# Performance work log

Hardware: AMD Instinct MI355X
Metric: run time of the kernel (lower is better)

Reference implementation:

```python
import jax, jax.numpy as jnp
import numpy as np

H = 8          # nheads
D_OUT = 1024   # tf_out_dim
D_HEAD = D_OUT // H
LN_EPS = 1e-5


def setup_inputs() -> dict:
    key = jax.random.key(0)
    ks = jax.random.split(key, 8)
    n_tok, d_in = 512, 1024
    return {
        "x": jax.random.normal(ks[0], (n_tok, d_in), jnp.float32),
        "c": jax.random.normal(ks[1], (H, n_tok, D_HEAD, D_HEAD), jnp.float32),
        "m_prev": jax.random.normal(ks[2], (H, n_tok, 1), jnp.float32),
        "n_prev": jax.random.normal(ks[3], (H, n_tok, D_HEAD), jnp.float32),
        "Wqkvo": jax.random.normal(ks[4], (d_in, 4 * D_OUT), jnp.float32) * 0.02,
        "bqkvo": jax.random.normal(ks[5], (4 * D_OUT,), jnp.float32) * 0.02,
        "Wuf": jax.random.normal(ks[6], (d_in, 2 * H), jnp.float32) * 0.02,
        "buf": jax.random.normal(ks[7], (2 * H,), jnp.float32) * 0.02,
    }


def reference(x, c, m_prev, n_prev, Wqkvo, bqkvo, Wuf, buf):
    n_tok = x.shape[0]
    scale = jnp.sqrt(jnp.float32(D_HEAD))  # sqrt(tf_out_dim / nheads)

    # projections: 'n (h d) -> h n d'
    qkvo = (x @ Wqkvo + bqkvo).reshape(n_tok, H, 4 * D_HEAD).transpose(1, 0, 2)
    q, k, v, o = jnp.split(qkvo, 4, axis=-1)          # each (H, n, d)
    k = k / scale

    # per-token outer-product update matrix ct = v k^T : (H, n, d, d)
    ct = v[..., :, None] * k[..., None, :]

    uf = (x @ Wuf + buf).reshape(n_tok, H, 2).transpose(1, 0, 2)  # (H, n, 2)
    u, f = uf[..., 0:1], uf[..., 1:2]                  # (H, n, 1)

    # stabilized exp gating (gate='exp', c is not None branch)
    m = jnp.maximum(f + m_prev, u)                     # (H, n, 1)
    ue = jnp.exp(u - m)
    fe = jnp.exp(f + m_prev - m)

    c_new = fe[..., None] * c + ue[..., None] * ct     # (H, n, d, d)
    n_new = fe * n_prev + ue * k                       # (H, n, d)

    # readout (note: original uses ct, not c_new, in the readout einsum)
    h = jnp.einsum('hnkl,hnl->hnk', ct, q)             # (H, n, d)
    nm = jnp.abs(jnp.einsum('hnk,hnk->hn', n_new, q))  # (H, n)
    h = h / jnp.maximum(nm, 1.0)[..., None]
    h = h * jax.nn.sigmoid(o)

    # 'h n d -> n (h d)', residual, LayerNorm over last dim (no affine)
    h = h.transpose(1, 0, 2).reshape(n_tok, D_OUT)
    h = x + h
    mu = jnp.mean(h, axis=-1, keepdims=True)
    var = jnp.var(h, axis=-1, keepdims=True)
    h = (h - mu) / jnp.sqrt(var + LN_EPS)
    return (c_new, h)
```

## Files before the change

kernel.cpp:

```cpp
#include <hip/hip_runtime.h>
#include <hip/hip_bf16.h>
#include <math.h>

#define KSCALE 0.08838834764831845f

typedef __bf16 bf16x8 __attribute__((ext_vector_type(8)));
typedef float  f32x4  __attribute__((ext_vector_type(4)));
typedef unsigned short u16x4 __attribute__((ext_vector_type(4)));
typedef unsigned short u16x8 __attribute__((ext_vector_type(8)));

__device__ inline unsigned short f2bf(float f) {
    unsigned int u = __float_as_uint(f);
    unsigned int r = (u + 0x7FFFu + ((u >> 16) & 1u)) >> 16;
    return (unsigned short)r;
}

__device__ __forceinline__ void gll16(const unsigned short* g, unsigned short* l) {
    __builtin_amdgcn_global_load_lds(
        (const __attribute__((address_space(1))) unsigned int*)g,
        (__attribute__((address_space(3))) unsigned int*)l,
        16, 0, 0);
}

__global__ __launch_bounds__(256) void prep_kernel(const float* __restrict__ x,
                                                   unsigned short* __restrict__ xb,
                                                   const float* __restrict__ W,
                                                   unsigned short* __restrict__ Wt,
                                                   const float* __restrict__ Wuf,
                                                   const float* __restrict__ buf,
                                                   const float* __restrict__ m_prev,
                                                   float* __restrict__ fe_ue) {
    int b = blockIdx.x;
    const int tid = threadIdx.x;
    if (b < 512) {
        int t = b * 256 + tid;
        float4 v = reinterpret_cast<const float4*>(x)[t];
        u16x4 o = { f2bf(v.x), f2bf(v.y), f2bf(v.z), f2bf(v.w) };
        reinterpret_cast<u16x4*>(xb)[t] = o;
    } else if (b < 1536) {
        __shared__ unsigned short tile[64][65];
        int bb = b - 512;
        int k0 = (bb & 15) * 64;
        int n0 = (bb >> 4) * 64;
        int r16 = tid >> 4, c4 = (tid & 15) * 4;
#pragma unroll
        for (int p = 0; p < 4; ++p) {
            int r = p * 16 + r16;
            float4 v = *reinterpret_cast<const float4*>(&W[(size_t)(k0 + r) * 4096 + n0 + c4]);
            tile[r][c4 + 0] = f2bf(v.x);
            tile[r][c4 + 1] = f2bf(v.y);
            tile[r][c4 + 2] = f2bf(v.z);
            tile[r][c4 + 3] = f2bf(v.w);
        }
        __syncthreads();
        int kc = (tid & 7) * 8, r32 = tid >> 3;
#pragma unroll
        for (int p = 0; p < 2; ++p) {
            int rr = p * 32 + r32;
            u16x8 o;
#pragma unroll
            for (int j = 0; j < 8; ++j) o[j] = tile[kc + j][rr];
            *reinterpret_cast<u16x8*>(&Wt[(size_t)(n0 + rr) * 1024 + k0 + kc]) = o;
        }
    } else {
        const int n = b - 1536;
        const int lane = tid & 63, w = tid >> 6;
        const float* xr = x + (size_t)n * 1024;
        float4 p = {0.f, 0.f, 0.f, 0.f};
#pragma unroll
        for (int i = 0; i < 16; ++i) {
            int k = lane + i * 64;
            float xv = xr[k];
            float4 wv = *reinterpret_cast<const float4*>(&Wuf[(size_t)k * 16 + 4 * w]);
            p.x += xv * wv.x; p.y += xv * wv.y; p.z += xv * wv.z; p.w += xv * wv.w;
        }
#pragma unroll
        for (int off = 32; off; off >>= 1) {
            p.x += __shfl_down(p.x, off);
            p.y += __shfl_down(p.y, off);
            p.z += __shfl_down(p.z, off);
            p.w += __shfl_down(p.w, off);
        }
        if (lane == 0) {
#pragma unroll
            for (int t = 0; t < 2; ++t) {
                int h = 2 * w + t;
                float u = (t ? p.z : p.x) + buf[4 * w + 2 * t];
                float f = (t ? p.w : p.y) + buf[4 * w + 2 * t + 1];
                float mp = m_prev[h * 512 + n];
                float m = fmaxf(f + mp, u);
                fe_ue[(h * 512 + n) * 2 + 0] = expf(f + mp - m);
                fe_ue[(h * 512 + n) * 2 + 1] = expf(u - m);
            }
        }
    }
}

__global__ __launch_bounds__(256) void gemm_qkvo(const unsigned short* __restrict__ A,
                                                 const unsigned short* __restrict__ Bt,
                                                 const float* __restrict__ bias,
                                                 float* __restrict__ C) {
    __shared__ __align__(16) unsigned short As[2][64 * 64];
    __shared__ __align__(16) unsigned short Bs[2][64 * 64];
    const int bn = blockIdx.x & 63;
    const int bm = blockIdx.x >> 6;
    const int m0 = bm * 64, n0 = bn * 64;
    const int tid = threadIdx.x;
    const int lane = tid & 63, wave = tid >> 6;
    const int wr = wave >> 1, wc = wave & 1;
    f32x4 acc[2][2] = {};

    const int srow = lane >> 3;
    const int scol = (lane & 7) * 8;

#pragma unroll
    for (int c = 0; c < 2; ++c) {
        int chunk = wave * 2 + c;
        int row = chunk * 8 + srow;
        gll16(A + (size_t)(m0 + row) * 1024 + scol, &As[0][chunk * 512]);
        gll16(Bt + (size_t)(n0 + row) * 1024 + scol, &Bs[0][chunk * 512]);
    }
    __syncthreads();

    int cur = 0;
    for (int t = 0; t < 16; ++t) {
        if (t < 15) {
            int k0 = (t + 1) * 64;
#pragma unroll
            for (int c = 0; c < 2; ++c) {
                int chunk = wave * 2 + c;
                int row = chunk * 8 + srow;
                gll16(A + (size_t)(m0 + row) * 1024 + k0 + scol, &As[cur ^ 1][chunk * 512]);
                gll16(Bt + (size_t)(n0 + row) * 1024 + k0 + scol, &Bs[cur ^ 1][chunk * 512]);
            }
        }
        const unsigned short* as = As[cur];
        const unsigned short* bs = Bs[cur];
        const int row = lane & 15;
        const int kof = (lane >> 4) * 8;
#pragma unroll
        for (int kk = 0; kk < 2; ++kk) {
            int kb = kk * 32 + kof;
            bf16x8 a0 = *reinterpret_cast<const bf16x8*>(&as[(wr * 32 + row) * 64 + kb]);
            bf16x8 a1 = *reinterpret_cast<const bf16x8*>(&as[(wr * 32 + 16 + row) * 64 + kb]);
            bf16x8 b0 = *reinterpret_cast<const bf16x8*>(&bs[(wc * 32 + row) * 64 + kb]);
            bf16x8 b1 = *reinterpret_cast<const bf16x8*>(&bs[(wc * 32 + 16 + row) * 64 + kb]);
            acc[0][0] = __builtin_amdgcn_mfma_f32_16x16x32_bf16(a0, b0, acc[0][0], 0, 0, 0);
            acc[0][1] = __builtin_amdgcn_mfma_f32_16x16x32_bf16(a0, b1, acc[0][1], 0, 0, 0);
            acc[1][0] = __builtin_amdgcn_mfma_f32_16x16x32_bf16(a1, b0, acc[1][0], 0, 0, 0);
            acc[1][1] = __builtin_amdgcn_mfma_f32_16x16x32_bf16(a1, b1, acc[1][1], 0, 0, 0);
        }
        __syncthreads();
        cur ^= 1;
    }

    const int cn = lane & 15, cm = (lane >> 4) * 4;
#pragma unroll
    for (int i = 0; i < 2; ++i)
#pragma unroll
        for (int j = 0; j < 2; ++j) {
            int gm = m0 + wr * 32 + i * 16 + cm;
            int gn = n0 + wc * 32 + j * 16 + cn;
            float b = bias[gn];
#pragma unroll
            for (int v = 0; v < 4; ++v)
                C[(size_t)(gm + v) * 4096 + gn] = acc[i][j][v] + b;
        }
}

__global__ __launch_bounds__(256) void fuse_main(const float* __restrict__ qkvo,
                                                 const float* __restrict__ c_in,
                                                 const float* __restrict__ n_prev,
                                                 const float* __restrict__ fe_ue,
                                                 float* __restrict__ c_out,
                                                 float* __restrict__ hst) {
    const int blk = blockIdx.x;
    const int h = blk >> 9, n = blk & 511;
    const int tid = threadIdx.x;
    __shared__ float k_s[128], v_s[128];
    __shared__ float rkq[4], rnq[4];

    const float* base = qkvo + (size_t)n * 4096 + h * 512;
    const float fe = fe_ue[(h * 512 + n) * 2 + 0];
    const float ue = fe_ue[(h * 512 + n) * 2 + 1];

    float kq_p = 0.f, nq_p = 0.f;
    if (tid < 128) {
        float q = base[tid];
        float k = base[128 + tid] * KSCALE;
        float v = base[256 + tid];
        k_s[tid] = k;
        v_s[tid] = v;
        float nn = fe * n_prev[(size_t)(h * 512 + n) * 128 + tid] + ue * k;
        kq_p = k * q;
        nq_p = nn * q;
    }
#pragma unroll
    for (int off = 32; off; off >>= 1) {
        kq_p += __shfl_down(kq_p, off);
        nq_p += __shfl_down(nq_p, off);
    }
    if ((tid & 63) == 0) { rkq[tid >> 6] = kq_p; rnq[tid >> 6] = nq_p; }
    __syncthreads();
    const float kq = rkq[0] + rkq[1];
    const float nm = fabsf(rnq[0] + rnq[1]);
    const float g = kq / fmaxf(nm, 1.0f);

    const f32x4* cin4 = reinterpret_cast<const f32x4*>(c_in + (size_t)(h * 512 + n) * 16384);
    f32x4* cout4 = reinterpret_cast<f32x4*>(c_out + (size_t)(h * 512 + n) * 16384);
#pragma unroll
    for (int it = 0; it < 16; ++it) {
        int e4 = tid + it * 256;
        int i = e4 >> 5;
        int j4 = (e4 & 31) * 4;
        f32x4 cv = __builtin_nontemporal_load(&cin4[e4]);
        float uv = ue * v_s[i];
        f32x4 o;
        o.x = fe * cv.x + uv * k_s[j4 + 0];
        o.y = fe * cv.y + uv * k_s[j4 + 1];
        o.z = fe * cv.z + uv * k_s[j4 + 2];
        o.w = fe * cv.w + uv * k_s[j4 + 3];
        __builtin_nontemporal_store(o, &cout4[e4]);
    }

    if (tid < 128) {
        float o = base[384 + tid];
        float sig = 1.f / (1.f + expf(-o));
        hst[(size_t)n * 1024 + h * 128 + tid] = v_s[tid] * g * sig;
    }
}

__global__ __launch_bounds__(256) void ln_kernel(const float* __restrict__ x,
                                                 const float* __restrict__ hst,
                                                 float* __restrict__ out) {
    int n = blockIdx.x, tid = threadIdx.x;
    float4 hv = reinterpret_cast<const float4*>(hst + (size_t)n * 1024)[tid];
    float4 xv = reinterpret_cast<const float4*>(x + (size_t)n * 1024)[tid];
    float4 s = { hv.x + xv.x, hv.y + xv.y, hv.z + xv.z, hv.w + xv.w };
    float sum = s.x + s.y + s.z + s.w;
    float sq = s.x * s.x + s.y * s.y + s.z * s.z + s.w * s.w;
#pragma unroll
    for (int off = 32; off; off >>= 1) {
        sum += __shfl_down(sum, off);
        sq += __shfl_down(sq, off);
    }
    __shared__ float rs[4], rq[4];
    if ((tid & 63) == 0) { rs[tid >> 6] = sum; rq[tid >> 6] = sq; }
    __syncthreads();
    sum = rs[0] + rs[1] + rs[2] + rs[3];
    sq = rq[0] + rq[1] + rq[2] + rq[3];
    float mu = sum * (1.f / 1024.f);
    float var = sq * (1.f / 1024.f) - mu * mu;
    float inv = rsqrtf(var + 1e-5f);
    float4 o4 = { (s.x - mu) * inv, (s.y - mu) * inv, (s.z - mu) * inv, (s.w - mu) * inv };
    reinterpret_cast<float4*>(out)[(size_t)n * 256 + tid] = o4;
}

extern "C" void kernel_launch(void* const* d_in, const int* in_sizes, int n_in,
                              void* d_out, int out_size, void* d_ws, size_t ws_size,
                              hipStream_t stream) {
    const float* x      = (const float*)d_in[0];
    const float* c_in   = (const float*)d_in[1];
    const float* m_prev = (const float*)d_in[2];
    const float* n_prev = (const float*)d_in[3];
    const float* Wqkvo  = (const float*)d_in[4];
    const float* bqkvo  = (const float*)d_in[5];
    const float* Wuf    = (const float*)d_in[6];
    const float* buf    = (const float*)d_in[7];
    float* out = (float*)d_out;
    char* ws = (char*)d_ws;

    unsigned short* xb   = (unsigned short*)(ws);
    unsigned short* Wt   = (unsigned short*)(ws + (1u << 20));
    float* qkvo          = (float*)(ws + 9u * (1u << 20));
    float* fe_ue         = (float*)(ws + 17u * (1u << 20));
    float* hst           = (float*)(ws + 17u * (1u << 20) + (1u << 16));

    prep_kernel<<<dim3(2048), dim3(256), 0, stream>>>(x, xb, Wqkvo, Wt, Wuf, buf, m_prev, fe_ue);
    gemm_qkvo  <<<dim3(512),  dim3(256), 0, stream>>>(xb, Wt, bqkvo, qkvo);
    fuse_main  <<<dim3(4096), dim3(256), 0, stream>>>(qkvo, c_in, n_prev, fe_ue, out, hst);
    ln_kernel  <<<dim3(512),  dim3(256), 0, stream>>>(x, hst, out + 67108864ull);
}
```

Measured before the change: 132.2 us.

## Split-K the QKVO GEMM and fuse LayerNorm into main kernel via counters

The projection GEMM is split into two K halves, so it launches 1024 blocks instead of 512 and writes two partial outputs. The main fused kernel sums the partials and adds the bias. The separate LayerNorm kernel is removed. The last of the 8 head-blocks for a token, found through an atomic counter, does the residual add and LayerNorm. This aims to raise GEMM occupancy and drop one launch and its tail, at the cost of extra partial-result traffic and atomic and fence overhead.

```diff
diff --git a/kernel.cpp b/kernel.cpp
--- a/kernel.cpp
+++ b/kernel.cpp
@@ -29,10 +29,12 @@
                                                    const float* __restrict__ Wuf,
                                                    const float* __restrict__ buf,
                                                    const float* __restrict__ m_prev,
-                                                   float* __restrict__ fe_ue) {
+                                                   float* __restrict__ fe_ue,
+                                                   int* __restrict__ cnt) {
     int b = blockIdx.x;
     const int tid = threadIdx.x;
     if (b < 512) {
+        if (b == 0) { cnt[tid] = 0; cnt[tid + 256] = 0; }
         int t = b * 256 + tid;
         float4 v = reinterpret_cast<const float4*>(x)[t];
         u16x4 o = { f2bf(v.x), f2bf(v.y), f2bf(v.z), f2bf(v.w) };
@@ -98,13 +100,16 @@
 
 __global__ __launch_bounds__(256) void gemm_qkvo(const unsigned short* __restrict__ A,
                                                  const unsigned short* __restrict__ Bt,
-                                                 const float* __restrict__ bias,
-                                                 float* __restrict__ C) {
+                                                 float* __restrict__ Cp) {
     __shared__ __align__(16) unsigned short As[2][64 * 64];
     __shared__ __align__(16) unsigned short Bs[2][64 * 64];
-    const int bn = blockIdx.x & 63;
-    const int bm = blockIdx.x >> 6;
+    const int kh = blockIdx.x >> 9;
+    const int t9 = blockIdx.x & 511;
+    const int bn = t9 & 63;
+    const int bm = t9 >> 6;
     const int m0 = bm * 64, n0 = bn * 64;
+    const size_t kb0 = (size_t)kh * 512;
+    float* C = Cp + (size_t)kh * (512 * 4096);
     const int tid = threadIdx.x;
     const int lane = tid & 63, wave = tid >> 6;
     const int wr = wave >> 1, wc = wave & 1;
@@ -117,15 +122,15 @@
     for (int c = 0; c < 2; ++c) {
         int chunk = wave * 2 + c;
         int row = chunk * 8 + srow;
-        gll16(A + (size_t)(m0 + row) * 1024 + scol, &As[0][chunk * 512]);
-        gll16(Bt + (size_t)(n0 + row) * 1024 + scol, &Bs[0][chunk * 512]);
+        gll16(A + (size_t)(m0 + row) * 1024 + kb0 + scol, &As[0][chunk * 512]);
+        gll16(Bt + (size_t)(n0 + row) * 1024 + kb0 + scol, &Bs[0][chunk * 512]);
     }
     __syncthreads();
 
     int cur = 0;
-    for (int t = 0; t < 16; ++t) {
-        if (t < 15) {
-            int k0 = (t + 1) * 64;
+    for (int t = 0; t < 8; ++t) {
+        if (t < 7) {
+            size_t k0 = kb0 + (t + 1) * 64;
 #pragma unroll
             for (int c = 0; c < 2; ++c) {
                 int chunk = wave * 2 + c;
@@ -161,34 +166,39 @@
         for (int j = 0; j < 2; ++j) {
             int gm = m0 + wr * 32 + i * 16 + cm;
             int gn = n0 + wc * 32 + j * 16 + cn;
-            float b = bias[gn];
 #pragma unroll
             for (int v = 0; v < 4; ++v)
-                C[(size_t)(gm + v) * 4096 + gn] = acc[i][j][v] + b;
+                C[(size_t)(gm + v) * 4096 + gn] = acc[i][j][v];
         }
 }
 
 __global__ __launch_bounds__(256) void fuse_main(const float* __restrict__ qkvo,
+                                                 const float* __restrict__ bias,
+                                                 const float* __restrict__ x,
                                                  const float* __restrict__ c_in,
                                                  const float* __restrict__ n_prev,
                                                  const float* __restrict__ fe_ue,
                                                  float* __restrict__ c_out,
-                                                 float* __restrict__ hst) {
+                                                 float* __restrict__ hst,
+                                                 int* __restrict__ cnt,
+                                                 float* __restrict__ h_out) {
     const int blk = blockIdx.x;
     const int h = blk >> 9, n = blk & 511;
     const int tid = threadIdx.x;
     __shared__ float k_s[128], v_s[128];
     __shared__ float rkq[4], rnq[4];
-
-    const float* base = qkvo + (size_t)n * 4096 + h * 512;
+    __shared__ int winflag;
+
+    const float* baseA = qkvo + (size_t)n * 4096 + h * 512;
+    const float* baseB = baseA + (size_t)512 * 4096;
     const float fe = fe_ue[(h * 512 + n) * 2 + 0];
     const float ue = fe_ue[(h * 512 + n) * 2 + 1];
 
     float kq_p = 0.f, nq_p = 0.f;
     if (tid < 128) {
-        float q = base[tid];
-        float k = base[128 + tid] * KSCALE;
-        float v = base[256 + tid];
+        float q = baseA[tid] + baseB[tid] + bias[h * 512 + tid];
+        float k = (baseA[128 + tid] + baseB[128 + tid] + bias[h * 512 + 128 + tid]) * KSCALE;
+        float v = baseA[256 + tid] + baseB[256 + tid] + bias[h * 512 + 256 + tid];
         k_s[tid] = k;
         v_s[tid] = v;
         float nn = fe * n_prev[(size_t)(h * 512 + n) * 128 + tid] + ue * k;
@@ -224,36 +234,44 @@
     }
 
     if (tid < 128) {
-        float o = base[384 + tid];
+        float o = baseA[384 + tid] + baseB[384 + tid] + bias[h * 512 + 384 + tid];
         float sig = 1.f / (1.f + expf(-o));
         hst[(size_t)n * 1024 + h * 128 + tid] = v_s[tid] * g * sig;
     }
-}
-
-__global__ __launch_bounds__(256) void ln_kernel(const float* __restrict__ x,
-                                                 const float* __restrict__ hst,
-                                                 float* __restrict__ out) {
-    int n = blockIdx.x, tid = threadIdx.x;
-    float4 hv = reinterpret_cast<const float4*>(hst + (size_t)n * 1024)[tid];
-    float4 xv = reinterpret_cast<const float4*>(x + (size_t)n * 1024)[tid];
-    float4 s = { hv.x + xv.x, hv.y + xv.y, hv.z + xv.z, hv.w + xv.w };
-    float sum = s.x + s.y + s.z + s.w;
-    float sq = s.x * s.x + s.y * s.y + s.z * s.z + s.w * s.w;
-#pragma unroll
-    for (int off = 32; off; off >>= 1) {
-        sum += __shfl_down(sum, off);
-        sq += __shfl_down(sq, off);
-    }
-    __shared__ float rs[4], rq[4];
-    if ((tid & 63) == 0) { rs[tid >> 6] = sum; rq[tid >> 6] = sq; }
+
     __syncthreads();
-    sum = rs[0] + rs[1] + rs[2] + rs[3];
-    sq = rq[0] + rq[1] + rq[2] + rq[3];
-    float mu = sum * (1.f / 1024.f);
-    float var = sq * (1.f / 1024.f) - mu * mu;
-    float inv = rsqrtf(var + 1e-5f);
-    float4 o4 = { (s.x - mu) * inv, (s.y - mu) * inv, (s.z - mu) * inv, (s.w - mu) * inv };
-    reinterpret_cast<float4*>(out)[(size_t)n * 256 + tid] = o4;
+    if (tid == 0) {
+        __threadfence();
+        int old = atomicAdd(&cnt[n], 1);
+        winflag = (old == 7);
+    }
+    __syncthreads();
+    if (winflag) {
+        __threadfence();
+        float hv[4];
+#pragma unroll
+        for (int j = 0; j < 4; ++j)
+            hv[j] = __hip_atomic_load(&hst[(size_t)n * 1024 + tid * 4 + j],
+                                      __ATOMIC_ACQUIRE, __HIP_MEMORY_SCOPE_AGENT);
+        float4 xv = reinterpret_cast<const float4*>(x + (size_t)n * 1024)[tid];
+        float s0 = hv[0] + xv.x, s1 = hv[1] + xv.y, s2 = hv[2] + xv.z, s3 = hv[3] + xv.w;
+        float sum = s0 + s1 + s2 + s3;
+        float sq = s0 * s0 + s1 * s1 + s2 * s2 + s3 * s3;
+#pragma unroll
+        for (int off = 32; off; off >>= 1) {
+            sum += __shfl_down(sum, off);
+            sq += __shfl_down(sq, off);
+        }
+        if ((tid & 63) == 0) { rkq[tid >> 6] = sum; rnq[tid >> 6] = sq; }
+        __syncthreads();
+        sum = rkq[0] + rkq[1] + rkq[2] + rkq[3];
+        sq = rnq[0] + rnq[1] + rnq[2] + rnq[3];
+        float mu = sum * (1.f / 1024.f);
+        float var = sq * (1.f / 1024.f) - mu * mu;
+        float inv = rsqrtf(var + 1e-5f);
+        float4 o4 = { (s0 - mu) * inv, (s1 - mu) * inv, (s2 - mu) * inv, (s3 - mu) * inv };
+        reinterpret_cast<float4*>(h_out)[(size_t)n * 256 + tid] = o4;
+    }
 }
 
 extern "C" void kernel_launch(void* const* d_in, const int* in_sizes, int n_in,
@@ -273,11 +291,12 @@
     unsigned short* xb   = (unsigned short*)(ws);
     unsigned short* Wt   = (unsigned short*)(ws + (1u << 20));
     float* qkvo          = (float*)(ws + 9u * (1u << 20));
-    float* fe_ue         = (float*)(ws + 17u * (1u << 20));
-    float* hst           = (float*)(ws + 17u * (1u << 20) + (1u << 16));
-
-    prep_kernel<<<dim3(2048), dim3(256), 0, stream>>>(x, xb, Wqkvo, Wt, Wuf, buf, m_prev, fe_ue);
-    gemm_qkvo  <<<dim3(512),  dim3(256), 0, stream>>>(xb, Wt, bqkvo, qkvo);
-    fuse_main  <<<dim3(4096), dim3(256), 0, stream>>>(qkvo, c_in, n_prev, fe_ue, out, hst);
-    ln_kernel  <<<dim3(512),  dim3(256), 0, stream>>>(x, hst, out + 67108864ull);
-}
+    float* fe_ue         = (float*)(ws + 25u * (1u << 20));
+    int*   cnt           = (int*)(ws + 25u * (1u << 20) + (1u << 15));
+    float* hst           = (float*)(ws + 25u * (1u << 20) + (1u << 16));
+
+    prep_kernel<<<dim3(2048), dim3(256), 0, stream>>>(x, xb, Wqkvo, Wt, Wuf, buf, m_prev, fe_ue, cnt);
+    gemm_qkvo  <<<dim3(1024), dim3(256), 0, stream>>>(xb, Wt, qkvo);
+    fuse_main  <<<dim3(4096), dim3(256), 0, stream>>>(qkvo, bqkvo, x, c_in, n_prev, fe_ue,
+                                                      out, hst, cnt, out + 67108864ull);
+}
```

Result: slower. 450.7 us (+241.0%).

## Split QKVO GEMM along K into two partial sums reduced in fuse kernel

Applied to the files above, without the earlier changes.

The QKVO GEMM is split into two K-halves, which doubles the grid from 512 to 1024 blocks so more of the GPU's compute units are occupied. Each half writes its own partial output buffer, and the bias add moves into fuse_main, which now sums the two partials plus the bias when it loads q/k/v/o. This trades extra global writes and reads of an 8 MB partial buffer, plus a larger workspace, for better GEMM occupancy.

```diff
diff --git a/kernel.cpp b/kernel.cpp
--- a/kernel.cpp
+++ b/kernel.cpp
@@ -98,13 +98,16 @@
 
 __global__ __launch_bounds__(256) void gemm_qkvo(const unsigned short* __restrict__ A,
                                                  const unsigned short* __restrict__ Bt,
-                                                 const float* __restrict__ bias,
-                                                 float* __restrict__ C) {
+                                                 float* __restrict__ Cp) {
     __shared__ __align__(16) unsigned short As[2][64 * 64];
     __shared__ __align__(16) unsigned short Bs[2][64 * 64];
-    const int bn = blockIdx.x & 63;
-    const int bm = blockIdx.x >> 6;
+    const int kh = blockIdx.x >> 9;
+    const int t9 = blockIdx.x & 511;
+    const int bn = t9 & 63;
+    const int bm = t9 >> 6;
     const int m0 = bm * 64, n0 = bn * 64;
+    const size_t kb0 = (size_t)kh * 512;
+    float* C = Cp + (size_t)kh * (512 * 4096);
     const int tid = threadIdx.x;
     const int lane = tid & 63, wave = tid >> 6;
     const int wr = wave >> 1, wc = wave & 1;
@@ -117,15 +120,15 @@
     for (int c = 0; c < 2; ++c) {
         int chunk = wave * 2 + c;
         int row = chunk * 8 + srow;
-        gll16(A + (size_t)(m0 + row) * 1024 + scol, &As[0][chunk * 512]);
-        gll16(Bt + (size_t)(n0 + row) * 1024 + scol, &Bs[0][chunk * 512]);
+        gll16(A + (size_t)(m0 + row) * 1024 + kb0 + scol, &As[0][chunk * 512]);
+        gll16(Bt + (size_t)(n0 + row) * 1024 + kb0 + scol, &Bs[0][chunk * 512]);
     }
     __syncthreads();
 
     int cur = 0;
-    for (int t = 0; t < 16; ++t) {
-        if (t < 15) {
-            int k0 = (t + 1) * 64;
+    for (int t = 0; t < 8; ++t) {
+        if (t < 7) {
+            size_t k0 = kb0 + (t + 1) * 64;
 #pragma unroll
             for (int c = 0; c < 2; ++c) {
                 int chunk = wave * 2 + c;
@@ -161,14 +164,14 @@
         for (int j = 0; j < 2; ++j) {
             int gm = m0 + wr * 32 + i * 16 + cm;
             int gn = n0 + wc * 32 + j * 16 + cn;
-            float b = bias[gn];
 #pragma unroll
             for (int v = 0; v < 4; ++v)
-                C[(size_t)(gm + v) * 4096 + gn] = acc[i][j][v] + b;
+                C[(size_t)(gm + v) * 4096 + gn] = acc[i][j][v];
         }
 }
 
 __global__ __launch_bounds__(256) void fuse_main(const float* __restrict__ qkvo,
+                                                 const float* __restrict__ bias,
                                                  const float* __restrict__ c_in,
                                                  const float* __restrict__ n_prev,
                                                  const float* __restrict__ fe_ue,
@@ -180,15 +183,16 @@
     __shared__ float k_s[128], v_s[128];
     __shared__ float rkq[4], rnq[4];
 
-    const float* base = qkvo + (size_t)n * 4096 + h * 512;
+    const float* baseA = qkvo + (size_t)n * 4096 + h * 512;
+    const float* baseB = baseA + (size_t)512 * 4096;
     const float fe = fe_ue[(h * 512 + n) * 2 + 0];
     const float ue = fe_ue[(h * 512 + n) * 2 + 1];
 
     float kq_p = 0.f, nq_p = 0.f;
     if (tid < 128) {
-        float q = base[tid];
-        float k = base[128 + tid] * KSCALE;
-        float v = base[256 + tid];
+        float q = baseA[tid] + baseB[tid] + bias[h * 512 + tid];
+        float k = (baseA[128 + tid] + baseB[128 + tid] + bias[h * 512 + 128 + tid]) * KSCALE;
+        float v = baseA[256 + tid] + baseB[256 + tid] + bias[h * 512 + 256 + tid];
         k_s[tid] = k;
         v_s[tid] = v;
         float nn = fe * n_prev[(size_t)(h * 512 + n) * 128 + tid] + ue * k;
@@ -224,7 +228,7 @@
     }
 
     if (tid < 128) {
-        float o = base[384 + tid];
+        float o = baseA[384 + tid] + baseB[384 + tid] + bias[h * 512 + 384 + tid];
         float sig = 1.f / (1.f + expf(-o));
         hst[(size_t)n * 1024 + h * 128 + tid] = v_s[tid] * g * sig;
     }
@@ -273,11 +277,11 @@
     unsigned short* xb   = (unsigned short*)(ws);
     unsigned short* Wt   = (unsigned short*)(ws + (1u << 20));
     float* qkvo          = (float*)(ws + 9u * (1u << 20));
-    float* fe_ue         = (float*)(ws + 17u * (1u << 20));
-    float* hst           = (float*)(ws + 17u * (1u << 20) + (1u << 16));
+    float* fe_ue         = (float*)(ws + 25u * (1u << 20));
+    float* hst           = (float*)(ws + 25u * (1u << 20) + (1u << 16));
 
     prep_kernel<<<dim3(2048), dim3(256), 0, stream>>>(x, xb, Wqkvo, Wt, Wuf, buf, m_prev, fe_ue);
-    gemm_qkvo  <<<dim3(512),  dim3(256), 0, stream>>>(xb, Wt, bqkvo, qkvo);
-    fuse_main  <<<dim3(4096), dim3(256), 0, stream>>>(qkvo, c_in, n_prev, fe_ue, out, hst);
+    gemm_qkvo  <<<dim3(1024), dim3(256), 0, stream>>>(xb, Wt, qkvo);
+    fuse_main  <<<dim3(4096), dim3(256), 0, stream>>>(qkvo, bqkvo, c_in, n_prev, fe_ue, out, hst);
     ln_kernel  <<<dim3(512),  dim3(256), 0, stream>>>(x, hst, out + 67108864ull);
 }
```

Result: faster. 129.5 us (-2.0%).
